# Kernel tuning notes

Measured on AMD Instinct MI355X. Metric: run time of the kernel, lower is better.

The kernel has to match this reference:

```python
import jax, jax.numpy as jnp
import numpy as np

HIDDEN = 1024
HEADS = 16
HEAD_DIM = HIDDEN // HEADS
B, S = 2, 2048


def setup_inputs() -> dict:
    key = jax.random.key(0)
    k1, k2, k3 = jax.random.split(key, 3)
    x = jax.random.normal(k1, (B, S, HIDDEN), dtype=jnp.float32)
    qkv_w = jax.random.normal(k2, (3 * HIDDEN, HIDDEN), dtype=jnp.float32) * (HIDDEN ** -0.5)
    out_w = jax.random.normal(k3, (HIDDEN, HIDDEN), dtype=jnp.float32) * (HIDDEN ** -0.5)
    return {"x": x, "qkv_w": qkv_w, "out_w": out_w}


def reference(x, qkv_w, out_w):
    b, s, d = x.shape
    scale = HEAD_DIM ** -0.5
    # qkv projection (Linear without bias: x @ W^T)
    qkv = x @ qkv_w.T                                   # [b, s, 3d]
    qkv = qkv.reshape(b, s, 3, HEADS, HEAD_DIM)
    qkv = jnp.transpose(qkv, (2, 0, 3, 1, 4))           # [3, b, h, s, hd]
    q, k, v = qkv[0] * scale, qkv[1], qkv[2]
    # causal attention (blocked torch loop == full causal softmax attention)
    scores = jnp.einsum('bhqd,bhkd->bhqk', q, k)        # [b, h, s, s]
    causal = jnp.tril(jnp.ones((s, s), dtype=bool))
    scores = jnp.where(causal[None, None], scores, -jnp.inf)
    weights = jax.nn.softmax(scores, axis=-1)
    attn = jnp.einsum('bhqk,bhkd->bhqd', weights, v)    # [b, h, s, hd]
    attn = jnp.transpose(attn, (0, 2, 1, 3)).reshape(b, s, d)
    return attn @ out_w.T
```

## Files before the change

### kernel.cpp

```cpp
#include <hip/hip_runtime.h>
#include <hip/hip_bf16.h>
#include <math.h>

#define HIDDEN 1024
#define HEADS 16
#define HDIM 64
#define BATCH 2
#define SEQ 2048
#define BHN (BATCH*HEADS)
#define MTOT (BATCH*SEQ)

typedef __attribute__((ext_vector_type(8))) short short8;
typedef __attribute__((ext_vector_type(4))) short short4v;
typedef __attribute__((ext_vector_type(4))) float floatx4;

#define GL2LDS(gsrc, ldst) __builtin_amdgcn_global_load_lds( \
    (const __attribute__((address_space(1))) void*)(gsrc), \
    (__attribute__((address_space(3))) void*)(ldst), 16, 0, 0)

__device__ __forceinline__ short f2bf(float f) {
  union { float f; unsigned u; } v; v.f = f;
  unsigned u = v.u;
  unsigned r = (u + 0x7fffu + ((u >> 16) & 1u)) >> 16;
  return (short)r;
}

__global__ __launch_bounds__(256) void cvt3_f32_bf16(
    const float* __restrict__ a, const float* __restrict__ b, const float* __restrict__ c,
    short* __restrict__ oa, short* __restrict__ ob, short* __restrict__ oc) {
  int i = blockIdx.x * 256 + threadIdx.x;
  const float* src; short* dst; int j;
  if (i < 1048576)      { src = a; dst = oa; j = i; }
  else if (i < 1835008) { src = b; dst = ob; j = i - 1048576; }
  else                  { src = c; dst = oc; j = i - 1835008; }
  float4 f = reinterpret_cast<const float4*>(src)[j];
  short4 o;
  o.x = f2bf(f.x); o.y = f2bf(f.y); o.z = f2bf(f.z); o.w = f2bf(f.w);
  reinterpret_cast<short4*>(dst)[j] = o;
}

template<int EPI, int BN>
__global__ __launch_bounds__(256) void gemm_bt(
    const short* __restrict__ A, const short* __restrict__ B,
    int M, int N, int K,
    float* __restrict__ outF,
    short* __restrict__ outQ, short* __restrict__ outK, short* __restrict__ outV)
{
  constexpr int WN = BN / 2;
  constexpr int NI = BN / 32;
  __shared__ __align__(16) short As[128*64];
  __shared__ __align__(16) short Bs[BN*64];
  const int tid = threadIdx.x;
  const int wv = tid >> 6;
  const int lane = tid & 63;
  const int l15 = lane & 15;
  const int quad = lane >> 4;
  const int swl = l15 & 7;
  const int wm = wv >> 1, wn = wv & 1;
  const int row0 = blockIdx.y * 128, col0 = blockIdx.x * BN;

  floatx4 acc[4][NI];
#pragma unroll
  for (int i = 0; i < 4; i++)
#pragma unroll
    for (int j = 0; j < NI; j++) acc[i][j] = (floatx4){0.f, 0.f, 0.f, 0.f};

  for (int k0 = 0; k0 < K; k0 += 64) {
#pragma unroll
    for (int rd = 0; rd < 4; ++rd) {
      int chunk = rd * 256 + tid;
      int r = chunk >> 3, c = ((chunk & 7) ^ (r & 7)) << 3;
      GL2LDS(A + (long)(row0 + r) * K + k0 + c, As + (rd * 256 + wv * 64) * 8);
    }
#pragma unroll
    for (int rd = 0; rd < BN / 32; ++rd) {
      int chunk = rd * 256 + tid;
      int r = chunk >> 3, c = ((chunk & 7) ^ (r & 7)) << 3;
      GL2LDS(B + (long)(col0 + r) * K + k0 + c, Bs + (rd * 256 + wv * 64) * 8);
    }
    __syncthreads();

    short8 af[4][2], bfr[NI][2];
#pragma unroll
    for (int mi = 0; mi < 4; mi++) {
      const short* ap = As + (wm * 64 + mi * 16 + l15) * 64;
#pragma unroll
      for (int kk = 0; kk < 2; kk++)
        af[mi][kk] = *(const short8*)(ap + (((kk * 4 + quad) ^ swl) << 3));
    }
#pragma unroll
    for (int ni = 0; ni < NI; ni++) {
      const short* bp = Bs + (wn * WN + ni * 16 + l15) * 64;
#pragma unroll
      for (int kk = 0; kk < 2; kk++)
        bfr[ni][kk] = *(const short8*)(bp + (((kk * 4 + quad) ^ swl) << 3));
    }
#pragma unroll
    for (int mi = 0; mi < 4; mi++)
#pragma unroll
      for (int ni = 0; ni < NI; ni++)
#pragma unroll
        for (int kk = 0; kk < 2; kk++)
          acc[mi][ni] = __builtin_amdgcn_mfma_f32_16x16x32_bf16(af[mi][kk], bfr[ni][kk], acc[mi][ni], 0, 0, 0);
    __syncthreads();
  }

  if (EPI == 2) {
#pragma unroll
    for (int mi = 0; mi < 4; mi++) {
      int rr = row0 + wm * 64 + mi * 16 + quad * 4;
#pragma unroll
      for (int ni = 0; ni < NI; ni++) {
        int cc = col0 + wn * WN + ni * 16 + l15;
#pragma unroll
        for (int r = 0; r < 4; r++)
          outF[(long)(rr + r) * N + cc] = acc[mi][ni][r];
      }
    }
  } else {
#pragma unroll
    for (int mi = 0; mi < 4; mi++) {
      int rowg = row0 + wm * 64 + mi * 16 + quad * 4;
#pragma unroll
      for (int ni = 0; ni < NI; ni++) {
        int j = col0 + wn * WN + ni * 16 + l15;
        int t = j >> 10;
        int rem = j & 1023;
        int h = rem >> 6, d = rem & 63;
#pragma unroll
        for (int r = 0; r < 4; r++) {
          int i = rowg + r;
          int b = i >> 11, s = i & 2047;
          int bh = b * HEADS + h;
          float v = acc[mi][ni][r];
          if (t == 0)      outQ[(bh * SEQ + s) * HDIM + d] = f2bf(v * 0.18033688011112042f);
          else if (t == 1) outK[(bh * SEQ + s) * HDIM + d] = f2bf(v);
          else             outV[(bh * HDIM + d) * SEQ + s] = f2bf(v);
        }
      }
    }
  }
}

__device__ __forceinline__ void stage_kv(const short* __restrict__ kg,
                                         const short* __restrict__ vT,
                                         int bh, int kt, short* KsB, short* VsB,
                                         int tid, int wv) {
#pragma unroll
  for (int i = 0; i < 4; ++i) {
    int slot = i * 128 + tid;
    int r = slot >> 3;
    int sc = ((slot & 7) ^ (r & 7)) << 3;
    GL2LDS(kg + (bh * SEQ + kt * 64 + r) * HDIM + sc, KsB + (i * 128 + wv * 64) * 8);
    GL2LDS(vT + (bh * HDIM + r) * SEQ + kt * 64 + sc, VsB + (i * 128 + wv * 64) * 8);
  }
}

__global__ __launch_bounds__(128, 2) void flash_attn(
    const short* __restrict__ qg, const short* __restrict__ kg,
    const short* __restrict__ vT, short* __restrict__ attn)
{
  __shared__ __align__(16) short Ks[2][64 * 64];
  __shared__ __align__(16) short Vs[2][64 * 64];

  const int tid = threadIdx.x;
  const int wv = tid >> 6, lane = tid & 63;
  const int l15 = lane & 15, quad = lane >> 4;
  const int bh = blockIdx.x;
  const int rt = 31 - (int)blockIdx.y;
  const int m0 = rt * 64 + wv * 32;
  const int swl = l15 & 7;

  short8 aq[2][2];
#pragma unroll
  for (int mi = 0; mi < 2; mi++) {
    const short* qp = qg + (long)(bh * SEQ + m0 + mi * 16 + l15) * HDIM + quad * 8;
    aq[mi][0] = *(const short8*)qp;
    aq[mi][1] = *(const short8*)(qp + 32);
  }

  const short ONE = (short)0x3F80;
  const short4v ones4 = {ONE, ONE, ONE, ONE};

  floatx4 o[2][4], lsum[2];
#pragma unroll
  for (int mi = 0; mi < 2; mi++) {
    lsum[mi] = (floatx4){0.f, 0.f, 0.f, 0.f};
#pragma unroll
    for (int nt = 0; nt < 4; nt++) o[mi][nt] = (floatx4){0.f, 0.f, 0.f, 0.f};
  }

  const int ntiles = rt + 1;
  stage_kv(kg, vT, bh, 0, Ks[0], Vs[0], tid, wv);

  for (int kt = 0; kt < ntiles; ++kt) {
    __syncthreads();
    const int buf = kt & 1;
    if (kt + 1 < ntiles)
      stage_kv(kg, vT, bh, kt + 1, Ks[buf ^ 1], Vs[buf ^ 1], tid, wv);

    const short* KsB = Ks[buf];
    const short* VsB = Vs[buf];

    floatx4 sc[2][4];
#pragma unroll
    for (int mi = 0; mi < 2; mi++)
#pragma unroll
      for (int nh = 0; nh < 4; nh++) sc[mi][nh] = (floatx4){0.f, 0.f, 0.f, 0.f};
#pragma unroll
    for (int nh = 0; nh < 4; nh++) {
      const short* kp = KsB + (nh * 16 + l15) * 64;
      short8 kf0 = *(const short8*)(kp + ((quad ^ swl) << 3));
      short8 kf1 = *(const short8*)(kp + (((4 + quad) ^ swl) << 3));
#pragma unroll
      for (int mi = 0; mi < 2; mi++) {
        sc[mi][nh] = __builtin_amdgcn_mfma_f32_16x16x32_bf16(kf0, aq[mi][0], sc[mi][nh], 0, 0, 0);
        sc[mi][nh] = __builtin_amdgcn_mfma_f32_16x16x32_bf16(kf1, aq[mi][1], sc[mi][nh], 0, 0, 0);
      }
    }

    short4v pa[2][4];
#pragma unroll
    for (int mi = 0; mi < 2; mi++) {
      const int qrow = m0 + mi * 16 + l15;
      const bool full = (kt * 64 + 63) <= (m0 + mi * 16);
#pragma unroll
      for (int nh = 0; nh < 4; nh++) {
        unsigned u[4];
#pragma unroll
        for (int r = 0; r < 4; r++) {
          float pe = __builtin_amdgcn_exp2f(sc[mi][nh][r]);
          if (!full) {
            const int kpos = kt * 64 + nh * 16 + quad * 4 + r;
            pe = (kpos <= qrow) ? pe : 0.f;
          }
          u[r] = __builtin_bit_cast(unsigned, pe) & 0xffff0000u;
        }
        uint2 w;
        w.x = (u[0] >> 16) | u[1];
        w.y = (u[2] >> 16) | u[3];
        pa[mi][nh] = __builtin_bit_cast(short4v, w);
      }
    }

#pragma unroll
    for (int kk = 0; kk < 4; kk++) {
      short4v bv[4];
#pragma unroll
      for (int nt = 0; nt < 4; nt++) {
        const int ch = (kk * 2 + (quad >> 1)) ^ swl;
        bv[nt] = *(const short4v*)(VsB + (nt * 16 + l15) * 64 + (ch << 3) + ((quad & 1) << 2));
      }
#pragma unroll
      for (int mi = 0; mi < 2; mi++) {
        lsum[mi] = __builtin_amdgcn_mfma_f32_16x16x16bf16_1k(pa[mi][kk], ones4, lsum[mi], 0, 0, 0);
#pragma unroll
        for (int nt = 0; nt < 4; nt++)
          o[mi][nt] = __builtin_amdgcn_mfma_f32_16x16x16bf16_1k(pa[mi][kk], bv[nt], o[mi][nt], 0, 0, 0);
      }
    }
  }

  const int b = bh >> 4, h = bh & 15;
#pragma unroll
  for (int mi = 0; mi < 2; mi++)
#pragma unroll
    for (int r = 0; r < 4; r++) {
      const float inv = 1.0f / lsum[mi][r];
      const int s = m0 + mi * 16 + quad * 4 + r;
#pragma unroll
      for (int nt = 0; nt < 4; nt++)
        attn[(long)(b * SEQ + s) * HIDDEN + h * HDIM + nt * 16 + l15] = f2bf(o[mi][nt][r] * inv);
    }
}

extern "C" void kernel_launch(void* const* d_in, const int* in_sizes, int n_in,
                              void* d_out, int out_size, void* d_ws, size_t ws_size,
                              hipStream_t stream) {
  const float* x     = (const float*)d_in[0];
  const float* qkv_w = (const float*)d_in[1];
  const float* out_w = (const float*)d_in[2];
  float* out = (float*)d_out;

  short* xb   = (short*)d_ws;
  short* wqb  = xb  + MTOT * HIDDEN;
  short* wob  = wqb + 3 * HIDDEN * HIDDEN;
  short* qB   = wob + HIDDEN * HIDDEN;
  short* kB   = qB  + BHN * SEQ * HDIM;
  short* vTB  = kB  + BHN * SEQ * HDIM;
  short* attn = vTB + BHN * SEQ * HDIM;

  cvt3_f32_bf16<<<dim3(8192), dim3(256), 0, stream>>>(x, qkv_w, out_w, xb, wqb, wob);

  gemm_bt<1, 128><<<dim3(3 * HIDDEN / 128, MTOT / 128), dim3(256), 0, stream>>>(
      xb, wqb, MTOT, 3 * HIDDEN, HIDDEN, nullptr, qB, kB, vTB);

  flash_attn<<<dim3(BHN, SEQ / 64), dim3(128), 0, stream>>>(qB, kB, vTB, attn);

  gemm_bt<2, 64><<<dim3(HIDDEN / 64, MTOT / 128), dim3(256), 0, stream>>>(
      attn, wob, MTOT, HIDDEN, HIDDEN, out, nullptr, nullptr, nullptr);
}
```

Measured before the change: 180.4 us.

## Split long causal attention row tiles across two blocks and combine partials

Reschedules flash attention so row tiles in the upper half of the sequence have their key range split between two blocks. Each block writes unnormalized partial outputs and row sums, and a new combine kernel merges them. Blocks are paired with short unsplit row tiles so every block does a similar amount of work. This reduces the longest per-block critical path and tail imbalance, at the cost of an extra kernel launch, extra memory traffic, and bf16 rounding of partial outputs.

```diff
diff --git a/kernel.cpp b/kernel.cpp
--- a/kernel.cpp
+++ b/kernel.cpp
@@ -23,6 +23,10 @@
   unsigned u = v.u;
   unsigned r = (u + 0x7fffu + ((u >> 16) & 1u)) >> 16;
   return (short)r;
+}
+__device__ __forceinline__ float bf2f(short s) {
+  unsigned u = ((unsigned)(unsigned short)s) << 16;
+  return __builtin_bit_cast(float, u);
 }
 
 __global__ __launch_bounds__(256) void cvt3_f32_bf16(
@@ -158,7 +162,8 @@
 
 __global__ __launch_bounds__(128, 2) void flash_attn(
     const short* __restrict__ qg, const short* __restrict__ kg,
-    const short* __restrict__ vT, short* __restrict__ attn)
+    const short* __restrict__ vT, short* __restrict__ attn,
+    short* __restrict__ partO, float* __restrict__ partL)
 {
   __shared__ __align__(16) short Ks[2][64 * 64];
   __shared__ __align__(16) short Vs[2][64 * 64];
@@ -166,10 +171,23 @@
   const int tid = threadIdx.x;
   const int wv = tid >> 6, lane = tid & 63;
   const int l15 = lane & 15, quad = lane >> 4;
-  const int bh = blockIdx.x;
-  const int rt = 31 - (int)blockIdx.y;
+  const int swl = l15 & 7;
+
+  const int g = blockIdx.x;
+  const int band = g / 96, j = g % 96;
+  int bh, rt, kt0, kt1, half = 0;
+  bool psplit;
+  if (j < 64) {
+    rt = 31 - band; bh = j >> 1; half = j & 1;
+    const int n = rt + 1, n0 = (n + 1) >> 1;
+    kt0 = half ? n0 : 0; kt1 = half ? n : n0;
+    psplit = true;
+  } else {
+    rt = 15 - band; bh = j - 64;
+    kt0 = 0; kt1 = rt + 1;
+    psplit = false;
+  }
   const int m0 = rt * 64 + wv * 32;
-  const int swl = l15 & 7;
 
   short8 aq[2][2];
 #pragma unroll
@@ -190,13 +208,14 @@
     for (int nt = 0; nt < 4; nt++) o[mi][nt] = (floatx4){0.f, 0.f, 0.f, 0.f};
   }
 
-  const int ntiles = rt + 1;
-  stage_kv(kg, vT, bh, 0, Ks[0], Vs[0], tid, wv);
-
-  for (int kt = 0; kt < ntiles; ++kt) {
+  const int nk = kt1 - kt0;
+  stage_kv(kg, vT, bh, kt0, Ks[0], Vs[0], tid, wv);
+
+  for (int i = 0; i < nk; ++i) {
+    const int kt = kt0 + i;
     __syncthreads();
-    const int buf = kt & 1;
-    if (kt + 1 < ntiles)
+    const int buf = i & 1;
+    if (i + 1 < nk)
       stage_kv(kg, vT, bh, kt + 1, Ks[buf ^ 1], Vs[buf ^ 1], tid, wv);
 
     const short* KsB = Ks[buf];
@@ -261,17 +280,60 @@
     }
   }
 
+  if (!psplit) {
+    const int b = bh >> 4, h = bh & 15;
+#pragma unroll
+    for (int mi = 0; mi < 2; mi++)
+#pragma unroll
+      for (int r = 0; r < 4; r++) {
+        const float inv = 1.0f / lsum[mi][r];
+        const int s = m0 + mi * 16 + quad * 4 + r;
+#pragma unroll
+        for (int nt = 0; nt < 4; nt++)
+          attn[(long)(b * SEQ + s) * HIDDEN + h * HDIM + nt * 16 + l15] = f2bf(o[mi][nt][r] * inv);
+      }
+  } else {
+    const int set = (bh * 16 + (rt - 16)) * 2 + half;
+    short* po = partO + (long)set * 4096;
+    float* pl = partL + set * 64;
+#pragma unroll
+    for (int mi = 0; mi < 2; mi++)
+#pragma unroll
+      for (int r = 0; r < 4; r++) {
+        const int qloc = wv * 32 + mi * 16 + quad * 4 + r;
+#pragma unroll
+        for (int nt = 0; nt < 4; nt++)
+          po[qloc * 64 + nt * 16 + l15] = f2bf(o[mi][nt][r]);
+        if (l15 == 0) pl[qloc] = lsum[mi][r];
+      }
+  }
+}
+
+__global__ __launch_bounds__(256) void combine(
+    const short* __restrict__ partO, const float* __restrict__ partL,
+    short* __restrict__ attn)
+{
+  const int g = blockIdx.x;
+  const int bh = g & 31, r16 = g >> 5;
+  const int rt = 16 + r16;
+  const int setA = (bh * 16 + r16) * 2;
+  const int row = threadIdx.x >> 2, seg = (threadIdx.x & 3) << 4;
+  const short* pa = partO + (long)setA * 4096 + row * 64 + seg;
+  const short* pb = pa + 4096;
+  const float inv = 1.0f / (partL[setA * 64 + row] + partL[(setA + 1) * 64 + row]);
   const int b = bh >> 4, h = bh & 15;
-#pragma unroll
-  for (int mi = 0; mi < 2; mi++)
-#pragma unroll
-    for (int r = 0; r < 4; r++) {
-      const float inv = 1.0f / lsum[mi][r];
-      const int s = m0 + mi * 16 + quad * 4 + r;
-#pragma unroll
-      for (int nt = 0; nt < 4; nt++)
-        attn[(long)(b * SEQ + s) * HIDDEN + h * HDIM + nt * 16 + l15] = f2bf(o[mi][nt][r] * inv);
-    }
+  const int s = rt * 64 + row;
+  short* dst = attn + (long)(b * SEQ + s) * HIDDEN + h * HDIM + seg;
+  short8 va0 = *(const short8*)pa, vb0 = *(const short8*)pb;
+  short8 va1 = *(const short8*)(pa + 8), vb1 = *(const short8*)(pb + 8);
+  short8 o0, o1;
+#pragma unroll
+  for (int i = 0; i < 8; i++) {
+    o0[i] = f2bf((bf2f(va0[i]) + bf2f(vb0[i])) * inv);
+    o1[i] = f2bf((bf2f(va1[i]) + bf2f(vb1[i])) * inv);
+  }
+  *(short8*)dst = o0;
+  *(short8*)(dst + 8) = o1;
 }
 
 extern "C" void kernel_launch(void* const* d_in, const int* in_sizes, int n_in,
@@ -282,20 +344,23 @@
   const float* out_w = (const float*)d_in[2];
   float* out = (float*)d_out;
 
-  short* xb   = (short*)d_ws;
-  short* wqb  = xb  + MTOT * HIDDEN;
-  short* wob  = wqb + 3 * HIDDEN * HIDDEN;
-  short* qB   = wob + HIDDEN * HIDDEN;
-  short* kB   = qB  + BHN * SEQ * HDIM;
-  short* vTB  = kB  + BHN * SEQ * HDIM;
-  short* attn = vTB + BHN * SEQ * HDIM;
+  short* xb    = (short*)d_ws;
+  short* wqb   = xb  + MTOT * HIDDEN;
+  short* wob   = wqb + 3 * HIDDEN * HIDDEN;
+  short* qB    = wob + HIDDEN * HIDDEN;
+  short* kB    = qB  + BHN * SEQ * HDIM;
+  short* vTB   = kB  + BHN * SEQ * HDIM;
+  short* attn  = vTB + BHN * SEQ * HDIM;
+  short* partO = attn + MTOT * HIDDEN;
+  float* partL = (float*)(partO + 1024 * 4096);
 
   cvt3_f32_bf16<<<dim3(8192), dim3(256), 0, stream>>>(x, qkv_w, out_w, xb, wqb, wob);
 
   gemm_bt<1, 128><<<dim3(3 * HIDDEN / 128, MTOT / 128), dim3(256), 0, stream>>>(
       xb, wqb, MTOT, 3 * HIDDEN, HIDDEN, nullptr, qB, kB, vTB);
 
-  flash_attn<<<dim3(BHN, SEQ / 64), dim3(128), 0, stream>>>(qB, kB, vTB, attn);
+  flash_attn<<<dim3(1536), dim3(128), 0, stream>>>(qB, kB, vTB, attn, partO, partL);
+  combine<<<dim3(512), dim3(256), 0, stream>>>(partO, partL, attn);
 
   gemm_bt<2, 64><<<dim3(HIDDEN / 64, MTOT / 128), dim3(256), 0, stream>>>(
       attn, wob, MTOT, HIDDEN, HIDDEN, out, nullptr, nullptr, nullptr);
```

After: 183.8 us. Within noise of the previous version (+1.9%).

## Load V directly to registers, use 32-wide MFMA for PV, raise occupancy

Applied to the files above, without the earlier changes.

The attention kernel no longer stages V through shared memory. Each lane loads its V fragments straight from global memory into registers, and the P·V and row-sum products use the 16x16x32 bf16 MFMA by joining two k-16 P fragments into one operand. Score computation now runs per mi to shrink live registers, launch bounds move to 4 blocks per CU, and the bf16 packing of P uses v_perm. The QKV epilogue also writes transposed V as packed short4 stores. The aim is to cut LDS traffic and instruction count and to raise occupancy, at the cost of uncoalesced or repeated global reads of V and some register pressure risk.

```diff
diff --git a/kernel.cpp b/kernel.cpp
--- a/kernel.cpp
+++ b/kernel.cpp
@@ -23,6 +23,9 @@
   unsigned u = v.u;
   unsigned r = (u + 0x7fffu + ((u >> 16) & 1u)) >> 16;
   return (short)r;
+}
+__device__ __forceinline__ short8 cat4(short4v a, short4v b) {
+  return __builtin_shufflevector(a, b, 0, 1, 2, 3, 4, 5, 6, 7);
 }
 
 __global__ __launch_bounds__(256) void cvt3_f32_bf16(
@@ -121,55 +124,59 @@
 #pragma unroll
     for (int mi = 0; mi < 4; mi++) {
       int rowg = row0 + wm * 64 + mi * 16 + quad * 4;
+      int b = rowg >> 11, s0 = rowg & 2047;
 #pragma unroll
       for (int ni = 0; ni < NI; ni++) {
         int j = col0 + wn * WN + ni * 16 + l15;
         int t = j >> 10;
         int rem = j & 1023;
         int h = rem >> 6, d = rem & 63;
-#pragma unroll
-        for (int r = 0; r < 4; r++) {
-          int i = rowg + r;
-          int b = i >> 11, s = i & 2047;
-          int bh = b * HEADS + h;
-          float v = acc[mi][ni][r];
-          if (t == 0)      outQ[(bh * SEQ + s) * HDIM + d] = f2bf(v * 0.18033688011112042f);
-          else if (t == 1) outK[(bh * SEQ + s) * HDIM + d] = f2bf(v);
-          else             outV[(bh * HDIM + d) * SEQ + s] = f2bf(v);
+        int bh = b * HEADS + h;
+        if (t == 2) {
+          short4 pk;
+          pk.x = f2bf(acc[mi][ni][0]); pk.y = f2bf(acc[mi][ni][1]);
+          pk.z = f2bf(acc[mi][ni][2]); pk.w = f2bf(acc[mi][ni][3]);
+          *(short4*)(outV + (long)(bh * HDIM + d) * SEQ + s0) = pk;
+        } else {
+#pragma unroll
+          for (int r = 0; r < 4; r++) {
+            float v = acc[mi][ni][r];
+            if (t == 0) outQ[(bh * SEQ + s0 + r) * HDIM + d] = f2bf(v * 0.18033688011112042f);
+            else        outK[(bh * SEQ + s0 + r) * HDIM + d] = f2bf(v);
+          }
         }
       }
     }
   }
 }
 
-__device__ __forceinline__ void stage_kv(const short* __restrict__ kg,
-                                         const short* __restrict__ vT,
-                                         int bh, int kt, short* KsB, short* VsB,
-                                         int tid, int wv) {
+__device__ __forceinline__ void stage_k(const short* __restrict__ kg,
+                                        int bh, int kt, short* KsB,
+                                        int tid, int wv) {
 #pragma unroll
   for (int i = 0; i < 4; ++i) {
     int slot = i * 128 + tid;
     int r = slot >> 3;
     int sc = ((slot & 7) ^ (r & 7)) << 3;
     GL2LDS(kg + (bh * SEQ + kt * 64 + r) * HDIM + sc, KsB + (i * 128 + wv * 64) * 8);
-    GL2LDS(vT + (bh * HDIM + r) * SEQ + kt * 64 + sc, VsB + (i * 128 + wv * 64) * 8);
-  }
-}
-
-__global__ __launch_bounds__(128, 2) void flash_attn(
+  }
+}
+
+__global__ __launch_bounds__(128, 4) void flash_attn(
     const short* __restrict__ qg, const short* __restrict__ kg,
     const short* __restrict__ vT, short* __restrict__ attn)
 {
   __shared__ __align__(16) short Ks[2][64 * 64];
-  __shared__ __align__(16) short Vs[2][64 * 64];
 
   const int tid = threadIdx.x;
   const int wv = tid >> 6, lane = tid & 63;
   const int l15 = lane & 15, quad = lane >> 4;
+  const int swl = l15 & 7;
   const int bh = blockIdx.x;
   const int rt = 31 - (int)blockIdx.y;
   const int m0 = rt * 64 + wv * 32;
-  const int swl = l15 & 7;
+
+  const short* vbase = vT + (long)bh * HDIM * SEQ;
 
   short8 aq[2][2];
 #pragma unroll
@@ -180,7 +187,7 @@
   }
 
   const short ONE = (short)0x3F80;
-  const short4v ones4 = {ONE, ONE, ONE, ONE};
+  const short8 ones8 = {ONE, ONE, ONE, ONE, ONE, ONE, ONE, ONE};
 
   floatx4 o[2][4], lsum[2];
 #pragma unroll
@@ -191,72 +198,71 @@
   }
 
   const int ntiles = rt + 1;
-  stage_kv(kg, vT, bh, 0, Ks[0], Vs[0], tid, wv);
+  stage_k(kg, bh, 0, Ks[0], tid, wv);
 
   for (int kt = 0; kt < ntiles; ++kt) {
     __syncthreads();
     const int buf = kt & 1;
+
+    short4v vlo[4][2], vhi[4][2];
+#pragma unroll
+    for (int nt = 0; nt < 4; nt++) {
+      const short* vp = vbase + (nt * 16 + l15) * SEQ + kt * 64 + quad * 4;
+#pragma unroll
+      for (int g32 = 0; g32 < 2; g32++) {
+        vlo[nt][g32] = *(const short4v*)(vp + g32 * 32);
+        vhi[nt][g32] = *(const short4v*)(vp + g32 * 32 + 16);
+      }
+    }
+
     if (kt + 1 < ntiles)
-      stage_kv(kg, vT, bh, kt + 1, Ks[buf ^ 1], Vs[buf ^ 1], tid, wv);
+      stage_k(kg, bh, kt + 1, Ks[buf ^ 1], tid, wv);
 
     const short* KsB = Ks[buf];
-    const short* VsB = Vs[buf];
-
-    floatx4 sc[2][4];
-#pragma unroll
-    for (int mi = 0; mi < 2; mi++)
-#pragma unroll
-      for (int nh = 0; nh < 4; nh++) sc[mi][nh] = (floatx4){0.f, 0.f, 0.f, 0.f};
-#pragma unroll
-    for (int nh = 0; nh < 4; nh++) {
-      const short* kp = KsB + (nh * 16 + l15) * 64;
-      short8 kf0 = *(const short8*)(kp + ((quad ^ swl) << 3));
-      short8 kf1 = *(const short8*)(kp + (((4 + quad) ^ swl) << 3));
-#pragma unroll
-      for (int mi = 0; mi < 2; mi++) {
-        sc[mi][nh] = __builtin_amdgcn_mfma_f32_16x16x32_bf16(kf0, aq[mi][0], sc[mi][nh], 0, 0, 0);
-        sc[mi][nh] = __builtin_amdgcn_mfma_f32_16x16x32_bf16(kf1, aq[mi][1], sc[mi][nh], 0, 0, 0);
-      }
-    }
-
-    short4v pa[2][4];
+
 #pragma unroll
     for (int mi = 0; mi < 2; mi++) {
+      floatx4 sc[4];
+#pragma unroll
+      for (int nh = 0; nh < 4; nh++) sc[nh] = (floatx4){0.f, 0.f, 0.f, 0.f};
+#pragma unroll
+      for (int nh = 0; nh < 4; nh++) {
+        const short* kp = KsB + (nh * 16 + l15) * 64;
+        short8 kf0 = *(const short8*)(kp + ((quad ^ swl) << 3));
+        short8 kf1 = *(const short8*)(kp + (((4 + quad) ^ swl) << 3));
+        sc[nh] = __builtin_amdgcn_mfma_f32_16x16x32_bf16(kf0, aq[mi][0], sc[nh], 0, 0, 0);
+        sc[nh] = __builtin_amdgcn_mfma_f32_16x16x32_bf16(kf1, aq[mi][1], sc[nh], 0, 0, 0);
+      }
+
+      short4v pa[4];
       const int qrow = m0 + mi * 16 + l15;
       const bool full = (kt * 64 + 63) <= (m0 + mi * 16);
 #pragma unroll
       for (int nh = 0; nh < 4; nh++) {
         unsigned u[4];
 #pragma unroll
-        for (int r = 0; r < 4; r++) {
-          float pe = __builtin_amdgcn_exp2f(sc[mi][nh][r]);
+        for (int r2 = 0; r2 < 4; r2++) {
+          float pe = __builtin_amdgcn_exp2f(sc[nh][r2]);
           if (!full) {
-            const int kpos = kt * 64 + nh * 16 + quad * 4 + r;
+            const int kpos = kt * 64 + nh * 16 + quad * 4 + r2;
             pe = (kpos <= qrow) ? pe : 0.f;
           }
-          u[r] = __builtin_bit_cast(unsigned, pe) & 0xffff0000u;
+          u[r2] = __builtin_bit_cast(unsigned, pe);
         }
         uint2 w;
-        w.x = (u[0] >> 16) | u[1];
-        w.y = (u[2] >> 16) | u[3];
-        pa[mi][nh] = __builtin_bit_cast(short4v, w);
-      }
-    }
-
-#pragma unroll
-    for (int kk = 0; kk < 4; kk++) {
-      short4v bv[4];
-#pragma unroll
-      for (int nt = 0; nt < 4; nt++) {
-        const int ch = (kk * 2 + (quad >> 1)) ^ swl;
-        bv[nt] = *(const short4v*)(VsB + (nt * 16 + l15) * 64 + (ch << 3) + ((quad & 1) << 2));
-      }
-#pragma unroll
-      for (int mi = 0; mi < 2; mi++) {
-        lsum[mi] = __builtin_amdgcn_mfma_f32_16x16x16bf16_1k(pa[mi][kk], ones4, lsum[mi], 0, 0, 0);
+        w.x = __builtin_amdgcn_perm(u[1], u[0], 0x07060302u);
+        w.y = __builtin_amdgcn_perm(u[3], u[2], 0x07060302u);
+        pa[nh] = __builtin_bit_cast(short4v, w);
+      }
+
+#pragma unroll
+      for (int g32 = 0; g32 < 2; g32++) {
+        const short8 a32 = cat4(pa[2 * g32], pa[2 * g32 + 1]);
+        lsum[mi] = __builtin_amdgcn_mfma_f32_16x16x32_bf16(a32, ones8, lsum[mi], 0, 0, 0);
 #pragma unroll
         for (int nt = 0; nt < 4; nt++)
-          o[mi][nt] = __builtin_amdgcn_mfma_f32_16x16x16bf16_1k(pa[mi][kk], bv[nt], o[mi][nt], 0, 0, 0);
+          o[mi][nt] = __builtin_amdgcn_mfma_f32_16x16x32_bf16(
+              a32, cat4(vlo[nt][g32], vhi[nt][g32]), o[mi][nt], 0, 0, 0);
       }
     }
   }
@@ -265,12 +271,12 @@
 #pragma unroll
   for (int mi = 0; mi < 2; mi++)
 #pragma unroll
-    for (int r = 0; r < 4; r++) {
-      const float inv = 1.0f / lsum[mi][r];
-      const int s = m0 + mi * 16 + quad * 4 + r;
+    for (int r2 = 0; r2 < 4; r2++) {
+      const float inv = 1.0f / lsum[mi][r2];
+      const int s = m0 + mi * 16 + quad * 4 + r2;
 #pragma unroll
       for (int nt = 0; nt < 4; nt++)
-        attn[(long)(b * SEQ + s) * HIDDEN + h * HDIM + nt * 16 + l15] = f2bf(o[mi][nt][r] * inv);
+        attn[(long)(b * SEQ + s) * HIDDEN + h * HDIM + nt * 16 + l15] = f2bf(o[mi][nt][r2] * inv);
     }
 }
 
```

Result: slower. 300.0 us (+66.3%).
